# Optimization experiments

Measured on AMD Instinct MI355X. Metric: run time of the kernel, lower is better.

## Reference

```python
import jax, jax.numpy as jnp
import numpy as np

DIM = 2048
NUM_EXPERTS = 8
EXPERT_DIM = 1024
B, S = 4, 2048


def setup_inputs() -> dict:
    key = jax.random.key(0)
    ks = jax.random.split(key, 8)
    sd = lambda fan_in: 1.0 / np.sqrt(fan_in)  # lecun-normal-ish init scale
    x = jax.random.normal(ks[0], (B, S, DIM), dtype=jnp.float32)
    Wr = jax.random.normal(ks[1], (DIM, NUM_EXPERTS), dtype=jnp.float32) * sd(DIM)
    br = jnp.zeros((NUM_EXPERTS,), dtype=jnp.float32)
    Wu = jax.random.normal(ks[2], (NUM_EXPERTS, DIM, EXPERT_DIM), dtype=jnp.float32) * sd(DIM)
    bu = jnp.zeros((NUM_EXPERTS, EXPERT_DIM), dtype=jnp.float32)
    Wd = jax.random.normal(ks[3], (NUM_EXPERTS, EXPERT_DIM, DIM), dtype=jnp.float32) * sd(EXPERT_DIM)
    bd = jnp.zeros((NUM_EXPERTS, DIM), dtype=jnp.float32)
    return {"x": x, "Wr": Wr, "br": br, "Wu": Wu, "bu": bu, "Wd": Wd, "bd": bd}


def reference(x, Wr, br, Wu, bu, Wd, bd):
    # Router: softmax over experts. x: [b,s,d]
    router_probs = jax.nn.softmax(jnp.einsum('bsd,de->bse', x, Wr) + br, axis=-1)
    # All experts as grouped GEMMs (e = expert axis).
    h = jnp.einsum('bsd,edf->bsef', x, Wu) + bu          # [b,s,e,expert_dim]
    h = jax.nn.gelu(h)                                    # tanh-approx gelu (flax default)
    y = jnp.einsum('bsef,efd->bsed', h, Wd) + bd          # [b,s,e,dim]
    out = jnp.einsum('bsed,bse->bsd', y, router_probs)    # router-weighted sum
    return out + x
```

## Files before the change

### kernel.cpp

```cpp
#include <hip/hip_runtime.h>
#include <stdint.h>

#define DIM   2048
#define NEXP  8
#define EDIM  1024
#define NTOK  8192

using bf16x8 = __attribute__((ext_vector_type(8))) short;
using f32x4  = __attribute__((ext_vector_type(4))) float;
using u16x2  = __attribute__((ext_vector_type(2))) unsigned short;

typedef __attribute__((address_space(3))) void lds_void_t;
typedef const __attribute__((address_space(1))) void gbl_void_t;

__device__ static inline void load_lds16(const void* g, void* l) {
    __builtin_amdgcn_global_load_lds((gbl_void_t*)g, (lds_void_t*)l, 16, 0, 0);
}

__device__ static inline unsigned short f2b(float x) {
    union { float f; unsigned u; } v; v.f = x;
    unsigned r = v.u + 0x7fffu + ((v.u >> 16) & 1u);
    return (unsigned short)(r >> 16);
}

__device__ static inline float gelu_f(float x) {
    float u = 0.7978845608028654f * x * (1.0f + 0.044715f * x * x);
    u = fminf(fmaxf(u, -15.0f), 15.0f);
    float e = __expf(2.0f * u);
    float th = (e - 1.0f) / (e + 1.0f);
    return 0.5f * x * (1.0f + th);
}

__global__ __launch_bounds__(256)
void transpose_cast(const float* __restrict__ in, unsigned short* __restrict__ out,
                    int R, int C) {
    __shared__ float tile[64][65];
    const size_t slab = (size_t)blockIdx.z * R * C;
    in  += slab;
    out += slab;
    const int r0 = blockIdx.y * 64;
    const int c0 = blockIdx.x * 64;
    const int tx = threadIdx.x & 63;
    const int tw = threadIdx.x >> 6;
    #pragma unroll
    for (int i = 0; i < 16; ++i)
        tile[tw * 16 + i][tx] = in[(size_t)(r0 + tw * 16 + i) * C + c0 + tx];
    __syncthreads();
    const int rp = (threadIdx.x & 31) * 2;
    const int cy = threadIdx.x >> 5;
    #pragma unroll
    for (int j = 0; j < 8; ++j) {
        const int c = cy + j * 8;
        u16x2 v;
        v.x = f2b(tile[rp][c]);
        v.y = f2b(tile[rp + 1][c]);
        *(u16x2*)&out[(size_t)(c0 + c) * R + r0 + rp] = v;
    }
}

__global__ __launch_bounds__(256)
void router_convert(const float* __restrict__ x, const float* __restrict__ Wr,
                    const float* __restrict__ br, unsigned short* __restrict__ xb,
                    float* __restrict__ probs) {
    const int t   = blockIdx.x;
    const int tid = threadIdx.x;
    const float* xr = x + (size_t)t * DIM;
    const float4* Wr4 = (const float4*)Wr;
    float s[NEXP];
    #pragma unroll
    for (int e = 0; e < NEXP; ++e) s[e] = 0.f;
    for (int j = tid; j < DIM; j += 256) {
        float v = xr[j];
        xb[(size_t)t * DIM + j] = f2b(v);
        const float4 w0 = Wr4[j * 2];
        const float4 w1 = Wr4[j * 2 + 1];
        s[0] += v * w0.x; s[1] += v * w0.y; s[2] += v * w0.z; s[3] += v * w0.w;
        s[4] += v * w1.x; s[5] += v * w1.y; s[6] += v * w1.z; s[7] += v * w1.w;
    }
    #pragma unroll
    for (int e = 0; e < NEXP; ++e)
        #pragma unroll
        for (int off = 32; off > 0; off >>= 1) s[e] += __shfl_down(s[e], off);
    __shared__ float part[4][NEXP];
    const int wave = tid >> 6, lane = tid & 63;
    if (lane == 0) {
        #pragma unroll
        for (int e = 0; e < NEXP; ++e) part[wave][e] = s[e];
    }
    __syncthreads();
    if (tid == 0) {
        float l[NEXP], mx = -1e30f;
        #pragma unroll
        for (int e = 0; e < NEXP; ++e) {
            l[e] = part[0][e] + part[1][e] + part[2][e] + part[3][e] + br[e];
            mx = fmaxf(mx, l[e]);
        }
        float sum = 0.f;
        #pragma unroll
        for (int e = 0; e < NEXP; ++e) { l[e] = __expf(l[e] - mx); sum += l[e]; }
        const float inv = 1.f / sum;
        #pragma unroll
        for (int e = 0; e < NEXP; ++e) probs[t * NEXP + e] = l[e] * inv;
    }
}

template <int MODE>
__global__ __launch_bounds__(256, 2)
void gemm_bt(const unsigned short* __restrict__ A,
             const unsigned short* __restrict__ Bt,
             int M, int N, int K,
             const float* __restrict__ probs,
             const float* __restrict__ bias,
             const float* __restrict__ xres,
             void* __restrict__ Cout)
{
    __shared__ unsigned short As[128 * 64];
    __shared__ unsigned short Bs[128 * 64];
    const int tid  = threadIdx.x;
    const int wave = tid >> 6;
    const int lane = tid & 63;
    const int wi = wave >> 1, wj = wave & 1;
    const int row0 = blockIdx.y * 128;
    const int col0 = blockIdx.x * 128;

    const unsigned short* pA[4];
    const unsigned short* pB[4];
    unsigned short* dA[4];
    unsigned short* dB[4];
    #pragma unroll
    for (int s = 0; s < 4; ++s) {
        const int g  = s * 256 + tid;
        const int r  = g >> 3;
        const int kc = (g & 7) ^ (r & 7);
        pA[s] = A  + (size_t)(row0 + r) * K + kc * 8;
        pB[s] = Bt + (size_t)(col0 + r) * K + kc * 8;
        dA[s] = &As[g * 8];
        dB[s] = &Bs[g * 8];
    }

    const int m = lane & 15;
    const int q = lane >> 4;
    const int xsw = m & 7;
    int aoff[4], boff[4], ko[2];
    #pragma unroll
    for (int t = 0; t < 4; ++t) {
        aoff[t] = (wi * 64 + t * 16 + m) * 64;
        boff[t] = (wj * 64 + t * 16 + m) * 64;
    }
    #pragma unroll
    for (int u = 0; u < 2; ++u)
        ko[u] = ((u * 4 + q) ^ xsw) * 8;

    f32x4 acc[4][4];
    #pragma unroll
    for (int i = 0; i < 4; ++i)
        #pragma unroll
        for (int j = 0; j < 4; ++j)
            acc[i][j] = (f32x4){0.f, 0.f, 0.f, 0.f};

    for (int k0 = 0; k0 < K; k0 += 64) {
        #pragma unroll
        for (int s = 0; s < 4; ++s) load_lds16(pA[s], dA[s]);
        #pragma unroll
        for (int s = 0; s < 4; ++s) load_lds16(pB[s], dB[s]);
        #pragma unroll
        for (int s = 0; s < 4; ++s) { pA[s] += 64; pB[s] += 64; }
        __syncthreads();
        #pragma unroll
        for (int u = 0; u < 2; ++u) {
            bf16x8 a[4], b[4];
            #pragma unroll
            for (int t = 0; t < 4; ++t)
                a[t] = *(const bf16x8*)&As[aoff[t] + ko[u]];
            #pragma unroll
            for (int t = 0; t < 4; ++t)
                b[t] = *(const bf16x8*)&Bs[boff[t] + ko[u]];
            #pragma unroll
            for (int i = 0; i < 4; ++i)
                #pragma unroll
                for (int j = 0; j < 4; ++j)
                    acc[i][j] = __builtin_amdgcn_mfma_f32_16x16x32_bf16(a[i], b[j], acc[i][j], 0, 0, 0);
        }
        __syncthreads();
    }

    if (MODE == 1) {
        unsigned short* H = (unsigned short*)Cout;
        const int e = col0 >> 10;
        #pragma unroll
        for (int i = 0; i < 4; ++i) {
            #pragma unroll
            for (int r = 0; r < 4; ++r) {
                const int rowg = row0 + wi * 64 + i * 16 + q * 4 + r;
                const float p = probs[rowg * NEXP + e];
                #pragma unroll
                for (int j = 0; j < 4; ++j) {
                    const int colg = col0 + wj * 64 + j * 16 + m;
                    float v = acc[i][j][r] + bias[colg];
                    H[(size_t)rowg * N + colg] = f2b(gelu_f(v) * p);
                }
            }
        }
    } else {
        float* O = (float*)Cout;
        #pragma unroll
        for (int i = 0; i < 4; ++i) {
            #pragma unroll
            for (int r = 0; r < 4; ++r) {
                const int rowg = row0 + wi * 64 + i * 16 + q * 4 + r;
                float p[NEXP];
                #pragma unroll
                for (int e = 0; e < NEXP; ++e) p[e] = probs[rowg * NEXP + e];
                #pragma unroll
                for (int j = 0; j < 4; ++j) {
                    const int colg = col0 + wj * 64 + j * 16 + m;
                    float v = acc[i][j][r];
                    #pragma unroll
                    for (int e = 0; e < NEXP; ++e) v += p[e] * bias[e * DIM + colg];
                    v += xres[(size_t)rowg * DIM + colg];
                    O[(size_t)rowg * N + colg] = v;
                }
            }
        }
    }
}

extern "C" void kernel_launch(void* const* d_in, const int* in_sizes, int n_in,
                              void* d_out, int out_size, void* d_ws, size_t ws_size,
                              hipStream_t stream) {
    const float* x  = (const float*)d_in[0];
    const float* Wr = (const float*)d_in[1];
    const float* br = (const float*)d_in[2];
    const float* Wu = (const float*)d_in[3];
    const float* bu = (const float*)d_in[4];
    const float* Wd = (const float*)d_in[5];
    const float* bd = (const float*)d_in[6];
    float* out = (float*)d_out;

    char* ws = (char*)d_ws;
    unsigned short* xb    = (unsigned short*)(ws);
    unsigned short* WuT   = (unsigned short*)(ws + 33554432);
    unsigned short* WdT   = (unsigned short*)(ws + 67108864);
    float*          probs = (float*)(ws + 100663296);
    unsigned short* h     = (unsigned short*)(ws + 100925440);

    transpose_cast<<<dim3(EDIM / 64, DIM / 64, NEXP), 256, 0, stream>>>(Wu, WuT, DIM, EDIM);
    transpose_cast<<<dim3(DIM / 64, (NEXP * EDIM) / 64, 1), 256, 0, stream>>>(Wd, WdT, NEXP * EDIM, DIM);
    router_convert<<<NTOK, 256, 0, stream>>>(x, Wr, br, xb, probs);
    gemm_bt<1><<<dim3((NEXP * EDIM) / 128, NTOK / 128), 256, 0, stream>>>(
        xb, WuT, NTOK, NEXP * EDIM, DIM, probs, bu, nullptr, h);
    gemm_bt<2><<<dim3(DIM / 128, NTOK / 128), 256, 0, stream>>>(
        h, WdT, NTOK, DIM, NEXP * EDIM, probs, bd, x, out);
}
```

Baseline: 792.1 us.

## Rewrite expert GEMMs as 256x256 tiles with double-buffered LDS pipeline

Replaces the 128x128 single-buffered GEMM with a 256x256 tile computed by 8 waves. LDS is double-buffered and global-to-LDS loads for the next k-tiles are interleaved between MFMA quarters, using explicit vmcnt waits, barriers and setprio. It also adds an XCD-aware block remap for L2 locality and hoists the bias and probability loads out of the epilogue loops. The risks are higher register pressure from 128 accumulator floats per lane, 64KB of LDS per block limiting occupancy, and fewer blocks for the down-projection GEMM (256 blocks).

New measurement: 791.0 us. No clear change (-0.1%).

```diff
diff --git a/kernel.cpp b/kernel.cpp
--- a/kernel.cpp
+++ b/kernel.cpp
@@ -104,8 +104,69 @@
     }
 }
 
+#define VMWAIT(n) asm volatile("s_waitcnt vmcnt(" #n ")" ::: "memory")
+#define FENCE_BARRIER() do { asm volatile("" ::: "memory"); \
+    __builtin_amdgcn_s_barrier(); asm volatile("" ::: "memory"); } while (0)
+
+#define STAGE_A(bufc, rho, koff) do { \
+    load_lds16(srcA + (size_t)((rho) * 128) * K + (koff),      dstA + (bufc) * 16384 + (rho) * 8192); \
+    load_lds16(srcA + (size_t)((rho) * 128 + 64) * K + (koff), dstA + (bufc) * 16384 + (rho) * 8192 + 4096); \
+} while (0)
+
+#define STAGE_B(bufc, rho, koff) do { \
+    load_lds16(srcB + (size_t)((rho) * 128) * K + (koff),      dstB + (bufc) * 16384 + (rho) * 8192); \
+    load_lds16(srcB + (size_t)((rho) * 128 + 64) * K + (koff), dstB + (bufc) * 16384 + (rho) * 8192 + 4096); \
+} while (0)
+
+#define RD_B(bb) \
+    _Pragma("unroll") for (int j = 0; j < 4; ++j) \
+    _Pragma("unroll") for (int u = 0; u < 2; ++u) \
+        bfr[j][u] = *(const bf16x8*)&Bs[bb][brow + j * 1024 + ko[u]];
+
+#define RD_A(dst, i0, bb) \
+    _Pragma("unroll") for (int ii = 0; ii < 2; ++ii) \
+    _Pragma("unroll") for (int u = 0; u < 2; ++u) \
+        dst[ii][u] = *(const bf16x8*)&As[bb][arow + ((i0) + ii) * 1024 + ko[u]];
+
+#define MFMA_Q(i0, AF) do { \
+    __builtin_amdgcn_s_setprio(1); \
+    _Pragma("unroll") for (int ii = 0; ii < 2; ++ii) \
+    _Pragma("unroll") for (int u = 0; u < 2; ++u) \
+    _Pragma("unroll") for (int j = 0; j < 4; ++j) \
+        acc[(i0) + ii][j] = __builtin_amdgcn_mfma_f32_16x16x32_bf16(AF[ii][u], bfr[j][u], acc[(i0) + ii][j], 0, 0, 0); \
+    __builtin_amdgcn_s_setprio(0); \
+} while (0)
+
+#define KTILE(bb, ISS1, ISS2, ISS3, ISS4, VMW) do { \
+    bf16x8 bfr[4][2], aA[2][2], aB[2][2]; \
+     \
+    RD_B(bb); RD_A(aA, 0, bb); RD_A(aB, 2, bb); \
+    ISS1; \
+    FENCE_BARRIER(); \
+    MFMA_Q(0, aA); \
+    FENCE_BARRIER(); \
+     \
+    RD_A(aA, 4, bb); \
+    ISS2; \
+    FENCE_BARRIER(); \
+    MFMA_Q(2, aB); \
+    FENCE_BARRIER(); \
+     \
+    RD_A(aB, 6, bb); \
+    ISS3; \
+    FENCE_BARRIER(); \
+    MFMA_Q(4, aA); \
+    FENCE_BARRIER(); \
+     \
+    ISS4; \
+    VMW; \
+    FENCE_BARRIER(); \
+    MFMA_Q(6, aB); \
+    FENCE_BARRIER(); \
+} while (0)
+
 template <int MODE>
-__global__ __launch_bounds__(256, 2)
+__global__ __launch_bounds__(512, 2)
 void gemm_bt(const unsigned short* __restrict__ A,
              const unsigned short* __restrict__ Bt,
              int M, int N, int K,
@@ -114,109 +175,107 @@
              const float* __restrict__ xres,
              void* __restrict__ Cout)
 {
-    __shared__ unsigned short As[128 * 64];
-    __shared__ unsigned short Bs[128 * 64];
+    __shared__ unsigned short As[2][16384];
+    __shared__ unsigned short Bs[2][16384];
+
     const int tid  = threadIdx.x;
     const int wave = tid >> 6;
     const int lane = tid & 63;
-    const int wi = wave >> 1, wj = wave & 1;
-    const int row0 = blockIdx.y * 128;
-    const int col0 = blockIdx.x * 128;
-
-    const unsigned short* pA[4];
-    const unsigned short* pB[4];
-    unsigned short* dA[4];
-    unsigned short* dB[4];
-    #pragma unroll
-    for (int s = 0; s < 4; ++s) {
-        const int g  = s * 256 + tid;
-        const int r  = g >> 3;
-        const int kc = (g & 7) ^ (r & 7);
-        pA[s] = A  + (size_t)(row0 + r) * K + kc * 8;
-        pB[s] = Bt + (size_t)(col0 + r) * K + kc * 8;
-        dA[s] = &As[g * 8];
-        dB[s] = &Bs[g * 8];
-    }
-
-    const int m = lane & 15;
-    const int q = lane >> 4;
-    const int xsw = m & 7;
-    int aoff[4], boff[4], ko[2];
-    #pragma unroll
-    for (int t = 0; t < 4; ++t) {
-        aoff[t] = (wi * 64 + t * 16 + m) * 64;
-        boff[t] = (wj * 64 + t * 16 + m) * 64;
-    }
-    #pragma unroll
-    for (int u = 0; u < 2; ++u)
-        ko[u] = ((u * 4 + q) ^ xsw) * 8;
-
-    f32x4 acc[4][4];
-    #pragma unroll
-    for (int i = 0; i < 4; ++i)
+    const int wm   = wave >> 2;
+    const int wn   = wave & 3;
+    const int m    = lane & 15;
+    const int q    = lane >> 4;
+    const int xsw  = m & 7;
+
+    const int nwg = gridDim.x * gridDim.y;
+    int bid = blockIdx.y * gridDim.x + blockIdx.x;
+    if (!(nwg & 7)) bid = (bid & 7) * (nwg >> 3) + (bid >> 3);
+    const int row0 = (bid / gridDim.x) * 256;
+    const int col0 = (bid % gridDim.x) * 256;
+
+    const int rloc = tid >> 3;
+    const int kc   = (tid & 7) ^ (rloc & 7);
+    const unsigned short* srcA = A  + (size_t)(row0 + rloc) * K + kc * 8;
+    const unsigned short* srcB = Bt + (size_t)(col0 + rloc) * K + kc * 8;
+    unsigned short* dstA = &As[0][0] + tid * 8;
+    unsigned short* dstB = &Bs[0][0] + tid * 8;
+
+    const int arow = (wm * 128 + m) * 64;
+    const int brow = (wn * 64  + m) * 64;
+    int ko[2];
+    #pragma unroll
+    for (int u = 0; u < 2; ++u) ko[u] = ((u * 4 + q) ^ xsw) * 8;
+
+    f32x4 acc[8][4];
+    #pragma unroll
+    for (int i = 0; i < 8; ++i)
         #pragma unroll
         for (int j = 0; j < 4; ++j)
             acc[i][j] = (f32x4){0.f, 0.f, 0.f, 0.f};
 
-    for (int k0 = 0; k0 < K; k0 += 64) {
-        #pragma unroll
-        for (int s = 0; s < 4; ++s) load_lds16(pA[s], dA[s]);
-        #pragma unroll
-        for (int s = 0; s < 4; ++s) load_lds16(pB[s], dB[s]);
-        #pragma unroll
-        for (int s = 0; s < 4; ++s) { pA[s] += 64; pB[s] += 64; }
-        __syncthreads();
-        #pragma unroll
-        for (int u = 0; u < 2; ++u) {
-            bf16x8 a[4], b[4];
-            #pragma unroll
-            for (int t = 0; t < 4; ++t)
-                a[t] = *(const bf16x8*)&As[aoff[t] + ko[u]];
-            #pragma unroll
-            for (int t = 0; t < 4; ++t)
-                b[t] = *(const bf16x8*)&Bs[boff[t] + ko[u]];
-            #pragma unroll
-            for (int i = 0; i < 4; ++i)
-                #pragma unroll
-                for (int j = 0; j < 4; ++j)
-                    acc[i][j] = __builtin_amdgcn_mfma_f32_16x16x32_bf16(a[i], b[j], acc[i][j], 0, 0, 0);
-        }
-        __syncthreads();
+    const int NT = K >> 6;
+
+    STAGE_B(0, 0, 0);  STAGE_B(0, 1, 0);  STAGE_A(0, 0, 0);  STAGE_A(0, 1, 0);
+    STAGE_B(1, 0, 64); STAGE_B(1, 1, 64); STAGE_A(1, 0, 64);
+    VMWAIT(6);
+    FENCE_BARRIER();
+
+    for (int t = 0; t + 3 < NT; t += 2) {
+        const size_t k1 = (size_t)(t + 1) * 64;
+        const size_t k2 = (size_t)(t + 2) * 64;
+        const size_t k3 = (size_t)(t + 3) * 64;
+        KTILE(0, STAGE_A(1, 1, k1), STAGE_B(0, 0, k2), STAGE_B(0, 1, k2), STAGE_A(0, 0, k2), VMWAIT(6));
+        KTILE(1, STAGE_A(0, 1, k2), STAGE_B(1, 0, k3), STAGE_B(1, 1, k3), STAGE_A(1, 0, k3), VMWAIT(6));
+    }
+    {
+        const size_t kl = (size_t)(NT - 1) * 64;
+        KTILE(0, STAGE_A(1, 1, kl), (void)0, (void)0, (void)0, VMWAIT(0));
+        KTILE(1, (void)0, (void)0, (void)0, (void)0, (void)0);
     }
 
     if (MODE == 1) {
         unsigned short* H = (unsigned short*)Cout;
         const int e = col0 >> 10;
-        #pragma unroll
-        for (int i = 0; i < 4; ++i) {
+        float bv[4];
+        #pragma unroll
+        for (int j = 0; j < 4; ++j) bv[j] = bias[col0 + wn * 64 + j * 16 + m];
+        #pragma unroll
+        for (int i = 0; i < 8; ++i) {
             #pragma unroll
             for (int r = 0; r < 4; ++r) {
-                const int rowg = row0 + wi * 64 + i * 16 + q * 4 + r;
+                const int rowg = row0 + wm * 128 + i * 16 + q * 4 + r;
                 const float p = probs[rowg * NEXP + e];
                 #pragma unroll
                 for (int j = 0; j < 4; ++j) {
-                    const int colg = col0 + wj * 64 + j * 16 + m;
-                    float v = acc[i][j][r] + bias[colg];
+                    const int colg = col0 + wn * 64 + j * 16 + m;
+                    float v = acc[i][j][r] + bv[j];
                     H[(size_t)rowg * N + colg] = f2b(gelu_f(v) * p);
                 }
             }
         }
     } else {
         float* O = (float*)Cout;
-        #pragma unroll
-        for (int i = 0; i < 4; ++i) {
+        float bdv[4][NEXP];
+        #pragma unroll
+        for (int j = 0; j < 4; ++j) {
+            const int colg = col0 + wn * 64 + j * 16 + m;
+            #pragma unroll
+            for (int e = 0; e < NEXP; ++e) bdv[j][e] = bias[e * DIM + colg];
+        }
+        #pragma unroll
+        for (int i = 0; i < 8; ++i) {
             #pragma unroll
             for (int r = 0; r < 4; ++r) {
-                const int rowg = row0 + wi * 64 + i * 16 + q * 4 + r;
+                const int rowg = row0 + wm * 128 + i * 16 + q * 4 + r;
                 float p[NEXP];
-                #pragma unroll
-                for (int e = 0; e < NEXP; ++e) p[e] = probs[rowg * NEXP + e];
+                *(float4*)&p[0] = *(const float4*)&probs[rowg * NEXP];
+                *(float4*)&p[4] = *(const float4*)&probs[rowg * NEXP + 4];
                 #pragma unroll
                 for (int j = 0; j < 4; ++j) {
-                    const int colg = col0 + wj * 64 + j * 16 + m;
+                    const int colg = col0 + wn * 64 + j * 16 + m;
                     float v = acc[i][j][r];
                     #pragma unroll
-                    for (int e = 0; e < NEXP; ++e) v += p[e] * bias[e * DIM + colg];
+                    for (int e = 0; e < NEXP; ++e) v += p[e] * bdv[j][e];
                     v += xres[(size_t)rowg * DIM + colg];
                     O[(size_t)rowg * N + colg] = v;
                 }
@@ -247,8 +306,8 @@
     transpose_cast<<<dim3(EDIM / 64, DIM / 64, NEXP), 256, 0, stream>>>(Wu, WuT, DIM, EDIM);
     transpose_cast<<<dim3(DIM / 64, (NEXP * EDIM) / 64, 1), 256, 0, stream>>>(Wd, WdT, NEXP * EDIM, DIM);
     router_convert<<<NTOK, 256, 0, stream>>>(x, Wr, br, xb, probs);
-    gemm_bt<1><<<dim3((NEXP * EDIM) / 128, NTOK / 128), 256, 0, stream>>>(
+    gemm_bt<1><<<dim3((NEXP * EDIM) / 256, NTOK / 256), 512, 0, stream>>>(
         xb, WuT, NTOK, NEXP * EDIM, DIM, probs, bu, nullptr, h);
-    gemm_bt<2><<<dim3(DIM / 128, NTOK / 128), 256, 0, stream>>>(
+    gemm_bt<2><<<dim3(DIM / 256, NTOK / 256), 512, 0, stream>>>(
         h, WdT, NTOK, DIM, NEXP * EDIM, probs, bd, x, out);
 }
```
